# Kernel optimization log

Measured on AMD Instinct MI355X. Metric: run time of the kernel, lower is better.

## Reference

```python
import jax, jax.numpy as jnp
import numpy as np

N_NODES = 20000
N_EDGES = 8192
UNITS = 128
NUM_GAUSSIANS = 50
CUTOFF = 8.0
GAMMA = 10.0
MIN_DIST, MAX_DIST = 0.0, 30.0


def setup_inputs() -> dict:
    key = jax.random.key(0)
    ks = jax.random.split(key, 6)
    node_features = jax.random.normal(ks[0], (N_NODES, UNITS), dtype=jnp.float32)
    edge_indices = jax.random.randint(ks[1], (2, N_EDGES), 0, N_NODES, dtype=jnp.int32)
    distances = jax.random.uniform(ks[2], (N_EDGES,), dtype=jnp.float32)
    # filter network params (Dense(units) -> swish -> Dense(units*units))
    W1 = jax.random.normal(ks[3], (NUM_GAUSSIANS, UNITS), dtype=jnp.float32) / np.sqrt(NUM_GAUSSIANS)
    b1 = jnp.zeros((UNITS,), dtype=jnp.float32)
    W2 = jax.random.normal(ks[4], (UNITS, UNITS * UNITS), dtype=jnp.float32) / np.sqrt(UNITS)
    b2 = jnp.zeros((UNITS * UNITS,), dtype=jnp.float32)
    # transform Dense(units, use_bias=False)
    Wt = jax.random.normal(ks[5], (UNITS, UNITS), dtype=jnp.float32) / np.sqrt(UNITS)
    return {"node_features": node_features, "edge_indices": edge_indices,
            "distances": distances, "W1": W1, "b1": b1, "W2": W2, "b2": b2, "Wt": Wt}


def reference(node_features, edge_indices, distances, W1, b1, W2, b2, Wt):
    n_nodes, units = node_features.shape
    # cutoff mask (multiplicative; dropped edges contribute zero to the scatter-sum,
    # equivalent to tf.boolean_mask + unsorted_segment_sum)
    mask = (distances <= CUTOFF).astype(node_features.dtype)  # [E]
    # Gaussian basis expansion
    centers = jnp.linspace(MIN_DIST, MAX_DIST, NUM_GAUSSIANS, dtype=jnp.float32)
    df = jnp.exp(-GAMMA * jnp.square(distances[:, None] - centers[None, :]))  # [E, G]
    # filter network: Dense -> swish -> Dense(units*units)
    h = jax.nn.silu(df @ W1 + b1)                    # [E, U]
    filters = (h @ W2 + b2).reshape(-1, units, units)  # [E, U, U]
    # gather source node features, transform, per-edge matvec
    src = node_features[edge_indices[0]]             # [E, U]
    transformed = src @ Wt                           # [E, U]
    filtered = jnp.einsum('eij,ej->ei', filters, transformed) * mask[:, None]  # [E, U]
    # scatter-sum to destination nodes
    messages = jax.ops.segment_sum(filtered, edge_indices[1], num_segments=n_nodes)
    return jax.nn.silu(messages)
```

## Files before the change

kernel.cpp:

```cpp
#include <hip/hip_runtime.h>
#include <hip/hip_fp16.h>


typedef _Float16 f16;
typedef __attribute__((ext_vector_type(8))) f16 f16x8;
typedef __attribute__((ext_vector_type(4))) float f32x4;
typedef __attribute__((ext_vector_type(4))) unsigned int u32x4;

#define NEDGE 8192
#define NNODE 20000
#define NG    50
#define KSTEPS 516
#define W2C_BYTES (KSTEPS * 8192)
#define HT_BYTES (64 * 132 * 128 * 2)
#define TM_BYTES (NEDGE * 128 * 2)
#define MSGH_BYTES (NNODE * 128 * 2)

#define LDS_H   0
#define LDS_TM  5120
#define LDS_TOT 37888

static __device__ __forceinline__ float fsilu(float x) { return x / (1.0f + __expf(-x)); }

static __device__ __forceinline__ void gll16(const void* g, void* l) {
  __builtin_amdgcn_global_load_lds(
      (const __attribute__((address_space(1))) unsigned int*)g,
      (__attribute__((address_space(3))) unsigned int*)l, 16, 0, 0);
}

__global__ __launch_bounds__(256) void k01(const float* __restrict__ W2,
                                           const float* __restrict__ b2,
                                           const float* __restrict__ NF,
                                           const int*   __restrict__ EI,
                                           const float* __restrict__ DI,
                                           const float* __restrict__ W1,
                                           const float* __restrict__ B1,
                                           const float* __restrict__ WT,
                                           f16* __restrict__ w2c,
                                           f16* __restrict__ ht2,
                                           f16* __restrict__ tmo,
                                           __half* __restrict__ msgh) {
  __shared__ union {
    f16 row[16384];
    struct {
      float df[16][NG]; float mask[16]; float src[16][128];
      float tt[16][132]; float ht[16][132];
    } k1;
  } sm;
  const int bid = blockIdx.x, tid = threadIdx.x;

  if (bid < 129) {
    const int u = bid;
    const float* src = (u < 128) ? (W2 + (size_t)u * 16384) : b2;
#pragma unroll
    for (int it = 0; it < 16; ++it) {
      int idx = it * 1024 + tid * 4;
      f32x4 v = *(const f32x4*)(src + idx);
#pragma unroll
      for (int r = 0; r < 4; ++r) sm.row[idx + r] = (f16)v[r];
    }
    __syncthreads();
#pragma unroll
    for (int q = 0; q < 8; ++q) {
      int fi = q * 256 + tid;
      int lane = fi & 63, nt = (fi >> 6) & 7, s = fi >> 9;
      int i = nt * 16 + (lane & 15);
      int j = s * 32 + (lane >> 4) * 8;
      u32x4 frag = *(const u32x4*)&sm.row[i * 128 + j];
      *((u32x4*)w2c + (size_t)(u * 4 + s) * 512 + nt * 64 + lane) = frag;
    }
    return;
  }
  if (bid < 641) {
    int et = bid - 129, e0 = et * 16;
    for (int idx = tid; idx < 16 * NG; idx += 256) {
      int e = idx / NG, g = idx - e * NG;
      float d = DI[e0 + e];
      float x = d - (float)g * (30.0f / 49.0f);
      sm.k1.df[e][g] = __expf(-10.0f * x * x);
    }
    if (tid < 16) sm.k1.mask[tid] = (DI[e0 + tid] <= 8.0f) ? 1.0f : 0.0f;
    for (int idx = tid; idx < 16 * 128; idx += 256) {
      int e = idx >> 7, u = idx & 127;
      sm.k1.src[e][u] = NF[(size_t)EI[e0 + e] * 128 + u];
    }
    __syncthreads();

    int j = tid & 127, es = tid >> 7;
    for (int e = es * 8; e < es * 8 + 8; ++e) {
      float acc = B1[j];
      for (int g = 0; g < NG; ++g) acc += sm.k1.df[e][g] * W1[g * 128 + j];
      sm.k1.ht[e][j] = fsilu(acc);
    }
    {
      float acc[8] = {0.f,0.f,0.f,0.f,0.f,0.f,0.f,0.f};
      for (int u = 0; u < 128; ++u) {
        float wv = WT[u * 128 + j];
#pragma unroll
        for (int e8 = 0; e8 < 8; ++e8) acc[e8] += sm.k1.src[es * 8 + e8][u] * wv;
      }
#pragma unroll
      for (int e8 = 0; e8 < 8; ++e8) sm.k1.tt[es * 8 + e8][j] = acc[e8];
    }
    __syncthreads();

    int eb = et >> 3, el0 = (et & 7) * 16;
    {
      int u = tid >> 1, hf = tid & 1;
      union { f16 s[8]; u32x4 v; } pk;
#pragma unroll
      for (int k = 0; k < 8; ++k) pk.s[k] = (f16)sm.k1.ht[hf * 8 + k][u];
      *(u32x4*)(ht2 + ((size_t)eb * 132 + u) * 128 + el0 + hf * 8) = pk.v;
    }
    if (tid < 16) ht2[((size_t)eb * 132 + 128) * 128 + el0 + tid] = (f16)1.0f;
    {
      int e = tid >> 4, cc = tid & 15;
      float m = sm.k1.mask[e];
      union { f16 s[8]; u32x4 v; } pk;
#pragma unroll
      for (int k = 0; k < 8; ++k) pk.s[k] = (f16)(m * sm.k1.tt[e][cc * 8 + k]);
      int col = (cc * 16) ^ ((e & 7) << 4);
      *(u32x4*)((char*)tmo + (size_t)(e0 + e) * 256 + col) = pk.v;
    }
    return;
  }
  {
    int base = (bid - 641) * 1024;
    u32x4 z = {0u, 0u, 0u, 0u};
#pragma unroll
    for (int k = 0; k < 4; ++k) {
      int i4 = base + k * 256 + tid;
      if (i4 < (MSGH_BYTES / 16)) ((u32x4*)msgh)[i4] = z;
    }
  }
}

__global__ __launch_bounds__(256, 2) void k2_gemm(const f16* __restrict__ w2c,
                                                  const f16* __restrict__ ht2,
                                                  const f16* __restrict__ tm,
                                                  const int* __restrict__ EI,
                                                  __half* __restrict__ msgh) {
  __shared__ u32x4 smem_v[LDS_TOT / 16];
  char* smem = (char*)smem_v;

  const int bid = blockIdx.x;
  const int c   = bid & 7;
  const int eb  = bid >> 3;
  const int e0  = eb * 128;
  const int nu  = (c == 7) ? 17 : 16;
  const int tid = threadIdx.x, w = tid >> 6, lane = tid & 63;
  const int l15 = lane & 15, g4 = lane >> 4;
  const int wm = w >> 1, wn = w & 1;

  {
    const char* tsrc = (const char*)tm + (size_t)e0 * 256 + w * 8192;
#pragma unroll
    for (int q = 0; q < 8; ++q)
      gll16(tsrc + q * 1024 + lane * 16,
            smem + LDS_TM + w * 8192 + q * 1024 + lane * 16);
  }
  if (w == 0) {
    const char* hsrc = (const char*)ht2 + ((size_t)eb * 132 + c * 16) * 256;
#pragma unroll
    for (int q = 0; q < 5; ++q)
      gll16(hsrc + q * 1024 + lane * 16, smem + LDS_H + q * 1024 + lane * 16);
  }
  __syncthreads();

  f16x8 Tall[4][4];
  {
    const int tmrow = LDS_TM + (wm * 64 + l15) * 256;
    const int colsw = (l15 & 7) << 4;
#pragma unroll
    for (int rt = 0; rt < 4; ++rt)
#pragma unroll
      for (int jc = 0; jc < 4; ++jc)
        Tall[rt][jc] = *(const f16x8*)(smem + tmrow + rt * 4096 +
                                       ((jc * 64 + g4 * 16) ^ colsw));
  }
  const __half* hbase = (const __half*)(smem + LDS_H) + wm * 64 + l15;

  __half2 hc[4], hn[4];
#pragma unroll
  for (int rt = 0; rt < 4; ++rt) hc[rt] = __half2half2(hbase[rt * 16]);

  const char* bp = (const char*)w2c + (size_t)(c * 64) * 8192 + wn * 4096 + lane * 16;
  f16x8 B0[4], B1[4];
#pragma unroll
  for (int nt = 0; nt < 4; ++nt) B0[nt] = *(const f16x8*)(bp + nt * 1024);
#pragma unroll
  for (int nt = 0; nt < 4; ++nt) B1[nt] = *(const f16x8*)(bp + 8192 + nt * 1024);
  size_t off = 2 * 8192;

  f32x4 acc[4][4];
#pragma unroll
  for (int rt = 0; rt < 4; ++rt)
#pragma unroll
    for (int nt = 0; nt < 4; ++nt) acc[rt][nt] = (f32x4){0.f, 0.f, 0.f, 0.f};

  for (int u = 0; u < nu; ++u) {
#pragma unroll
    for (int jc = 0; jc < 4; ++jc) {
      if (jc == 1) {
#pragma unroll
        for (int rt = 0; rt < 4; ++rt)
          hn[rt] = __half2half2(hbase[(u + 1) * 128 + rt * 16]);
      }
      union uf { f16x8 v; __half2 h[4]; };
      uf a[4];
#pragma unroll
      for (int rt = 0; rt < 4; ++rt) {
        uf t; t.v = Tall[rt][jc];
#pragma unroll
        for (int q = 0; q < 4; ++q) a[rt].h[q] = __hmul2(t.h[q], hc[rt]);
      }
      __builtin_amdgcn_s_setprio(1);
#pragma unroll
      for (int nt = 0; nt < 4; ++nt) {
        if ((jc & 1) == 0) {
#pragma unroll
          for (int rt = 0; rt < 4; ++rt)
            acc[rt][nt] = __builtin_amdgcn_mfma_f32_16x16x32_f16(a[rt].v, B0[nt], acc[rt][nt], 0, 0, 0);
          B0[nt] = *(const f16x8*)(bp + off + nt * 1024);
        } else {
#pragma unroll
          for (int rt = 0; rt < 4; ++rt)
            acc[rt][nt] = __builtin_amdgcn_mfma_f32_16x16x32_f16(a[rt].v, B1[nt], acc[rt][nt], 0, 0, 0);
          B1[nt] = *(const f16x8*)(bp + off + nt * 1024);
        }
      }
      __builtin_amdgcn_s_setprio(0);
      off += 8192;
    }
#pragma unroll
    for (int rt = 0; rt < 4; ++rt) hc[rt] = hn[rt];
  }

  const int* dst = EI + NEDGE;
#pragma unroll
  for (int rt = 0; rt < 4; ++rt) {
#pragma unroll
    for (int r = 0; r < 4; ++r) {
      int e = e0 + wm * 64 + rt * 16 + g4 * 4 + r;
      size_t rowb = (size_t)dst[e] * 128 + wn * 64;
#pragma unroll
      for (int nt = 0; nt < 4; ++nt) {
        float v  = acc[rt][nt][r];
        float pv = __shfl_xor(v, 1, 64);
        if ((l15 & 1) == 0) {
          __half2 h2;
          h2.x = __float2half_rn(v);
          h2.y = __float2half_rn(pv);
          unsigned int d = *(unsigned int*)&h2;
          unsigned long long addr =
              (unsigned long long)(msgh + rowb + nt * 16 + l15);
          asm volatile("global_atomic_pk_add_f16 %0, %1, off"
                       :: "v"(addr), "v"(d) : "memory");
        }
      }
    }
  }
}

__global__ __launch_bounds__(256) void k3_silu(const __half* __restrict__ msgh,
                                               float* __restrict__ out, int n8) {
  int idx = blockIdx.x * 256 + threadIdx.x;
  if (idx >= n8) return;
  union { u32x4 v; __half h[8]; } r;
  r.v = *(const u32x4*)(msgh + (size_t)idx * 8);
  f32x4 o0, o1;
#pragma unroll
  for (int cc = 0; cc < 4; ++cc) {
    o0[cc] = fsilu(__half2float(r.h[cc]));
    o1[cc] = fsilu(__half2float(r.h[4 + cc]));
  }
  *(f32x4*)(out + (size_t)idx * 8)     = o0;
  *(f32x4*)(out + (size_t)idx * 8 + 4) = o1;
}

extern "C" void kernel_launch(void* const* d_in, const int* in_sizes, int n_in,
                              void* d_out, int out_size, void* d_ws, size_t ws_size,
                              hipStream_t stream) {
  const float* NF = (const float*)d_in[0];
  const int*   EI = (const int*)  d_in[1];
  const float* DI = (const float*)d_in[2];
  const float* W1 = (const float*)d_in[3];
  const float* B1 = (const float*)d_in[4];
  const float* W2 = (const float*)d_in[5];
  const float* B2 = (const float*)d_in[6];
  const float* WT = (const float*)d_in[7];
  float* out = (float*)d_out;

  f16*    w2c  = (f16*)d_ws;
  f16*    ht2  = (f16*)((char*)d_ws + W2C_BYTES);
  f16*    tmo  = (f16*)((char*)d_ws + W2C_BYTES + HT_BYTES);
  __half* msgh = (__half*)((char*)d_ws + W2C_BYTES + HT_BYTES + TM_BYTES);
  size_t needed = (size_t)W2C_BYTES + HT_BYTES + TM_BYTES + MSGH_BYTES;
  if (ws_size < needed) return;

  k01    <<<dim3(954),  dim3(256), 0, stream>>>(W2, B2, NF, EI, DI, W1, B1, WT,
                                                w2c, ht2, tmo, msgh);
  k2_gemm<<<dim3(512),  dim3(256), 0, stream>>>(w2c, ht2, tmo, EI, msgh);
  k3_silu<<<dim3(1250), dim3(256), 0, stream>>>(msgh, out, NNODE * 128 / 8);
}
```

Measured before the change: 94.66 us.

## Replace fp16 packed atomics with fp32 partial buffer plus reduce kernel

The GEMM now writes each block's fp32 partial results per column chunk into a workspace buffer instead of doing packed fp16 atomics into a half-precision message array. A new reduce kernel sums the 8 chunks per edge and does fp32 atomics straight into the output, and SiLU runs in place on the output. The goal is fewer and less contended atomic operations and fp32 accumulation, at the cost of an extra kernel and about 32MB of partial writes and reads. If the workspace is too small it falls back to direct fp32 atomics.

Result: faster. 85.18 us (-10.0%).

```diff
diff --git a/kernel.cpp b/kernel.cpp
--- a/kernel.cpp
+++ b/kernel.cpp
@@ -14,7 +14,7 @@
 #define W2C_BYTES (KSTEPS * 8192)
 #define HT_BYTES (64 * 132 * 128 * 2)
 #define TM_BYTES (NEDGE * 128 * 2)
-#define MSGH_BYTES (NNODE * 128 * 2)
+#define FP_BYTES ((size_t)8 * NEDGE * 128 * 4)
 
 #define LDS_H   0
 #define LDS_TM  5120
@@ -39,7 +39,7 @@
                                            f16* __restrict__ w2c,
                                            f16* __restrict__ ht2,
                                            f16* __restrict__ tmo,
-                                           __half* __restrict__ msgh) {
+                                           float* __restrict__ out, int nz4) {
   __shared__ union {
     f16 row[16384];
     struct {
@@ -126,20 +126,22 @@
   }
   {
     int base = (bid - 641) * 1024;
-    u32x4 z = {0u, 0u, 0u, 0u};
+    f32x4 z = {0.f, 0.f, 0.f, 0.f};
 #pragma unroll
     for (int k = 0; k < 4; ++k) {
       int i4 = base + k * 256 + tid;
-      if (i4 < (MSGH_BYTES / 16)) ((u32x4*)msgh)[i4] = z;
-    }
-  }
-}
-
+      if (i4 < nz4) ((f32x4*)out)[i4] = z;
+    }
+  }
+}
+
+template<int MODE>
 __global__ __launch_bounds__(256, 2) void k2_gemm(const f16* __restrict__ w2c,
                                                   const f16* __restrict__ ht2,
                                                   const f16* __restrict__ tm,
                                                   const int* __restrict__ EI,
-                                                  __half* __restrict__ msgh) {
+                                                  float* __restrict__ fpart,
+                                                  float* __restrict__ msg) {
   __shared__ u32x4 smem_v[LDS_TOT / 16];
   char* smem = (char*)smem_v;
 
@@ -236,46 +238,63 @@
     for (int rt = 0; rt < 4; ++rt) hc[rt] = hn[rt];
   }
 
-  const int* dst = EI + NEDGE;
-#pragma unroll
-  for (int rt = 0; rt < 4; ++rt) {
-#pragma unroll
-    for (int r = 0; r < 4; ++r) {
-      int e = e0 + wm * 64 + rt * 16 + g4 * 4 + r;
-      size_t rowb = (size_t)dst[e] * 128 + wn * 64;
-#pragma unroll
-      for (int nt = 0; nt < 4; ++nt) {
-        float v  = acc[rt][nt][r];
-        float pv = __shfl_xor(v, 1, 64);
-        if ((l15 & 1) == 0) {
-          __half2 h2;
-          h2.x = __float2half_rn(v);
-          h2.y = __float2half_rn(pv);
-          unsigned int d = *(unsigned int*)&h2;
-          unsigned long long addr =
-              (unsigned long long)(msgh + rowb + nt * 16 + l15);
-          asm volatile("global_atomic_pk_add_f16 %0, %1, off"
-                       :: "v"(addr), "v"(d) : "memory");
-        }
-      }
-    }
-  }
-}
-
-__global__ __launch_bounds__(256) void k3_silu(const __half* __restrict__ msgh,
-                                               float* __restrict__ out, int n8) {
+  if (MODE == 0) {
+#pragma unroll
+    for (int rt = 0; rt < 4; ++rt) {
+#pragma unroll
+      for (int r = 0; r < 4; ++r) {
+        int e = e0 + wm * 64 + rt * 16 + g4 * 4 + r;
+        float* prow = fpart + ((size_t)c * NEDGE + e) * 128 + wn * 64 + l15;
+#pragma unroll
+        for (int nt = 0; nt < 4; ++nt)
+          prow[nt * 16] = acc[rt][nt][r];
+      }
+    }
+  } else {
+    const int* dst = EI + NEDGE;
+#pragma unroll
+    for (int rt = 0; rt < 4; ++rt) {
+#pragma unroll
+      for (int r = 0; r < 4; ++r) {
+        int e = e0 + wm * 64 + rt * 16 + g4 * 4 + r;
+        float* row = msg + (size_t)dst[e] * 128 + wn * 64 + l15;
+#pragma unroll
+        for (int nt = 0; nt < 4; ++nt)
+          atomicAdd(row + nt * 16, acc[rt][nt][r]);
+      }
+    }
+  }
+}
+
+__global__ __launch_bounds__(256) void k4_reduce(const float* __restrict__ fp,
+                                                 const int* __restrict__ EI,
+                                                 float* __restrict__ out) {
+  int gid = blockIdx.x * 256 + threadIdx.x;
+  int e  = gid >> 5;
+  int i0 = (gid & 31) << 2;
+  f32x4 s = {0.f, 0.f, 0.f, 0.f};
+#pragma unroll
+  for (int cc = 0; cc < 8; ++cc) {
+    f32x4 v = *(const f32x4*)(fp + ((size_t)cc * NEDGE + e) * 128 + i0);
+    s[0] += v[0]; s[1] += v[1]; s[2] += v[2]; s[3] += v[3];
+  }
+  float* row = out + (size_t)EI[NEDGE + e] * 128 + i0;
+  atomicAdd(row + 0, s[0]);
+  atomicAdd(row + 1, s[1]);
+  atomicAdd(row + 2, s[2]);
+  atomicAdd(row + 3, s[3]);
+}
+
+__global__ __launch_bounds__(256) void k3_silu(float* __restrict__ out, int n4) {
   int idx = blockIdx.x * 256 + threadIdx.x;
-  if (idx >= n8) return;
-  union { u32x4 v; __half h[8]; } r;
-  r.v = *(const u32x4*)(msgh + (size_t)idx * 8);
-  f32x4 o0, o1;
-#pragma unroll
-  for (int cc = 0; cc < 4; ++cc) {
-    o0[cc] = fsilu(__half2float(r.h[cc]));
-    o1[cc] = fsilu(__half2float(r.h[4 + cc]));
-  }
-  *(f32x4*)(out + (size_t)idx * 8)     = o0;
-  *(f32x4*)(out + (size_t)idx * 8 + 4) = o1;
+  int stride = gridDim.x * 256;
+  f32x4* p = (f32x4*)out;
+  for (; idx < n4; idx += stride) {
+    f32x4 v = p[idx];
+#pragma unroll
+    for (int cc = 0; cc < 4; ++cc) v[cc] = fsilu(v[cc]);
+    p[idx] = v;
+  }
 }
 
 extern "C" void kernel_launch(void* const* d_in, const int* in_sizes, int n_in,
@@ -291,15 +310,23 @@
   const float* WT = (const float*)d_in[7];
   float* out = (float*)d_out;
 
-  f16*    w2c  = (f16*)d_ws;
-  f16*    ht2  = (f16*)((char*)d_ws + W2C_BYTES);
-  f16*    tmo  = (f16*)((char*)d_ws + W2C_BYTES + HT_BYTES);
-  __half* msgh = (__half*)((char*)d_ws + W2C_BYTES + HT_BYTES + TM_BYTES);
-  size_t needed = (size_t)W2C_BYTES + HT_BYTES + TM_BYTES + MSGH_BYTES;
-  if (ws_size < needed) return;
-
-  k01    <<<dim3(954),  dim3(256), 0, stream>>>(W2, B2, NF, EI, DI, W1, B1, WT,
-                                                w2c, ht2, tmo, msgh);
-  k2_gemm<<<dim3(512),  dim3(256), 0, stream>>>(w2c, ht2, tmo, EI, msgh);
-  k3_silu<<<dim3(1250), dim3(256), 0, stream>>>(msgh, out, NNODE * 128 / 8);
-}
+  f16*   w2c = (f16*)d_ws;
+  f16*   ht2 = (f16*)((char*)d_ws + W2C_BYTES);
+  f16*   tmo = (f16*)((char*)d_ws + W2C_BYTES + HT_BYTES);
+  float* fp  = (float*)((char*)d_ws + W2C_BYTES + HT_BYTES + TM_BYTES);
+  size_t need_min  = (size_t)W2C_BYTES + HT_BYTES + TM_BYTES;
+  size_t need_fast = need_min + FP_BYTES;
+  if (ws_size < need_min) return;
+  const bool fast = (ws_size >= need_fast);
+
+  int nz4 = out_size / 4;
+  k01<<<dim3(1266), dim3(256), 0, stream>>>(W2, B2, NF, EI, DI, W1, B1, WT,
+                                            w2c, ht2, tmo, out, nz4);
+  if (fast) {
+    k2_gemm<0><<<dim3(512),  dim3(256), 0, stream>>>(w2c, ht2, tmo, EI, fp, out);
+    k4_reduce <<<dim3(1024), dim3(256), 0, stream>>>(fp, EI, out);
+  } else {
+    k2_gemm<1><<<dim3(512),  dim3(256), 0, stream>>>(w2c, ht2, tmo, EI, fp, out);
+  }
+  k3_silu<<<dim3(1024), dim3(256), 0, stream>>>(out, nz4);
+}
```
